# Kernel optimization log

Measured on AMD Instinct MI355X. Metric: run time of the kernel, lower is better.

Reference implementation:

```python
import jax, jax.numpy as jnp
import numpy as np

NEG_SLOPE_ATT = 0.2   # PyG GATConv attention leaky_relu slope
NEG_SLOPE_ACT = 0.01  # F.leaky_relu default between layers


def gat_conv(h, W, a_src, a_dst, b, src, dst, n_nodes):
    """Single-head PyG GATConv (concat, heads=1), self-loops already in src/dst."""
    h = h @ W                                     # [N, out]
    s = h @ a_src                                 # [N] per-node src attention logit
    d = h @ a_dst                                 # [N] per-node dst attention logit
    e = jax.nn.leaky_relu(s[src] + d[dst], negative_slope=NEG_SLOPE_ATT)  # [E']
    # numerically stable segment softmax over edges grouped by dst
    m = jax.ops.segment_max(e, dst, num_segments=n_nodes)
    ex = jnp.exp(e - jax.lax.stop_gradient(m)[dst])
    denom = jax.ops.segment_sum(ex, dst, num_segments=n_nodes)
    alpha = ex / denom[dst]                       # [E']
    out = jax.ops.segment_sum(h[src] * alpha[:, None], dst, num_segments=n_nodes)
    return out + b


def setup_inputs() -> dict:
    key = jax.random.key(0)
    ks = jax.random.split(key, 12)
    N, E, D, H, O, G = 50000, 800000, 128, 128, 64, 256
    x = jax.random.normal(ks[0], (N, D), dtype=jnp.float32)
    edge_index = jax.random.randint(ks[1], (2, E), 0, N, dtype=jnp.int64)
    batch = jnp.sort(jax.random.randint(ks[2], (N,), 0, G, dtype=jnp.int64))
    def glorot(k, shape):
        fan = sum(shape) if len(shape) > 1 else shape[0]
        return jax.random.normal(k, shape, dtype=jnp.float32) * np.float32(np.sqrt(2.0 / fan))
    return {
        "x": x, "edge_index": edge_index, "batch": batch, "n_graphs": G,
        "W1": glorot(ks[3], (D, H)), "a_src1": glorot(ks[4], (H,)), "a_dst1": glorot(ks[5], (H,)),
        "b1": jnp.zeros((H,), dtype=jnp.float32),
        "W2": glorot(ks[6], (H, O)), "a_src2": glorot(ks[7], (O,)), "a_dst2": glorot(ks[8], (O,)),
        "b2": jnp.zeros((O,), dtype=jnp.float32),
    }


def reference(x, edge_index, batch, n_graphs, W1, a_src1, a_dst1, b1, W2, a_src2, a_dst2, b2):
    N = x.shape[0]
    loops = jnp.arange(N, dtype=edge_index.dtype)
    src = jnp.concatenate([edge_index[0], loops])  # add self-loops (GATConv default)
    dst = jnp.concatenate([edge_index[1], loops])
    h = gat_conv(x, W1, a_src1, a_dst1, b1, src, dst, N)
    h = jax.nn.leaky_relu(h, negative_slope=NEG_SLOPE_ACT)  # dropout is identity in eval
    node_emb = gat_conv(h, W2, a_src2, a_dst2, b2, src, dst, N)
    # global_mean_pool
    sums = jax.ops.segment_sum(node_emb, batch, num_segments=n_graphs)
    counts = jax.ops.segment_sum(jnp.ones((N,), dtype=node_emb.dtype), batch, num_segments=n_graphs)
    return sums / jnp.maximum(counts, 1.0)[:, None]
```

## Files before the change

kernel.cpp:

```cpp
#include <hip/hip_runtime.h>

#define NEG_ATT 0.2f
#define NEG_ACT 0.01f

typedef short bf16x8 __attribute__((ext_vector_type(8)));
typedef float f32x4 __attribute__((ext_vector_type(4)));

__device__ __forceinline__ float lrelu(float x, float sl) { return x > 0.0f ? x : x * sl; }

__device__ __forceinline__ unsigned short f2bf(float f) {
  unsigned u = __float_as_uint(f);
  u = u + 0x7FFFu + ((u >> 16) & 1u);
  return (unsigned short)(u >> 16);
}
__device__ __forceinline__ float bf2f(unsigned short h) {
  return __uint_as_float(((unsigned)h) << 16);
}
__device__ __forceinline__ unsigned fenc(float f) {
  unsigned u = __float_as_uint(f);
  return u ^ ((unsigned)((int)u >> 31) | 0x80000000u);
}
__device__ __forceinline__ float fdec(unsigned e) {
  unsigned u = (e & 0x80000000u) ? (e ^ 0x80000000u) : ~e;
  return __uint_as_float(u);
}

#define BIN_CHUNK 4096
#define SLAB_CAP 4096
#define GEMM_LDS 34848

__global__ void prep_w_kernel(const float* __restrict__ W1, const float* __restrict__ W2,
                              unsigned short* __restrict__ w1h, unsigned short* __restrict__ w1l,
                              unsigned short* __restrict__ w2h, unsigned short* __restrict__ w2l,
                              int* __restrict__ bcur, unsigned* __restrict__ maxenc,
                              int NB, int H, int O) {
  int idx = blockIdx.x * 256 + threadIdx.x;
  if (idx < NB) bcur[idx] = 0;
  if (idx == NB) { maxenc[0] = 0u; maxenc[1] = 0u; }
  int n1 = 128 * H;
  const float* W; unsigned short *hi, *lo; int FOUT;
  if (idx < n1) {
    W = W1; hi = w1h; lo = w1l; FOUT = H;
  } else {
    idx -= n1;
    if (idx >= 128 * O) return;
    W = W2; hi = w2h; lo = w2l; FOUT = O;
  }
  int k = idx / FOUT, n = idx % FOUT;
  float w = W[idx];
  unsigned short h = f2bf(w);
  unsigned short l = f2bf(w - bf2f(h));
  int dst = ((k >> 3) * FOUT + n) * 8 + (k & 7);
  hi[dst] = h;
  lo[dst] = l;
}

__device__ __forceinline__ void binA_body(char* smem, const int* __restrict__ src,
                                          const int* __restrict__ dst, int* __restrict__ bcur,
                                          unsigned* __restrict__ pairs, int E, int NB) {
  int* hist = (int*)smem;
  int* cur = hist + 512;
  int tid = threadIdx.x;
  for (int t = tid; t < NB; t += 256) hist[t] = 0;
  __syncthreads();
  int base = blockIdx.x * BIN_CHUNK;
  int s[16], d[16];
#pragma unroll
  for (int i = 0; i < 16; ++i) {
    int idx = base + i * 256 + tid;
    s[i] = 0; d[i] = -1;
    if (idx < E) {
      s[i] = src[idx];
      d[i] = dst[idx];
      atomicAdd(&hist[d[i] >> 7], 1);
    }
  }
  __syncthreads();
  for (int t = tid; t < NB; t += 256) cur[t] = atomicAdd(&bcur[t], hist[t]);
  __syncthreads();
#pragma unroll
  for (int i = 0; i < 16; ++i) {
    if (d[i] >= 0) {
      int b = d[i] >> 7;
      int pos = atomicAdd(&cur[b], 1);
      if (pos < SLAB_CAP)
        pairs[(size_t)b * SLAB_CAP + pos] = (unsigned)s[i] | ((unsigned)(d[i] & 127) << 17);
    }
  }
}

template <int FOUT>
__device__ __forceinline__ void gemm_body(
    char* smem, const float* __restrict__ X, const unsigned short* __restrict__ Wh,
    const unsigned short* __restrict__ Wl,
    const float* __restrict__ asrc, const float* __restrict__ adst,
    unsigned short* __restrict__ Ho, float* __restrict__ So, float* __restrict__ Do,
    unsigned* __restrict__ maxslot, int N, int rowbase) {
  constexpr int NCB = FOUT / 16;
  unsigned short* Ah = (unsigned short*)smem;
  unsigned short* Al = Ah + 64 * 136;
  float* smaxw = (float*)(smem + 2 * 64 * 136 * 2);
  int tid = threadIdx.x;
#pragma unroll
  for (int i = 0; i < 8; ++i) {
    int idx = i * 256 + tid;
    int r = idx >> 5, c4 = (idx & 31) << 2;
    float4 v = make_float4(0.f, 0.f, 0.f, 0.f);
    if (rowbase + r < N) v = *(const float4*)(X + (size_t)(rowbase + r) * 128 + c4);
    ushort4 hv, lv;
    hv.x = f2bf(v.x); lv.x = f2bf(v.x - bf2f(hv.x));
    hv.y = f2bf(v.y); lv.y = f2bf(v.y - bf2f(hv.y));
    hv.z = f2bf(v.z); lv.z = f2bf(v.z - bf2f(hv.z));
    hv.w = f2bf(v.w); lv.w = f2bf(v.w - bf2f(hv.w));
    *(ushort4*)&Ah[r * 136 + c4] = hv;
    *(ushort4*)&Al[r * 136 + c4] = lv;
  }
  __syncthreads();
  int wave = tid >> 6, lane = tid & 63;
  int n15 = lane & 15, bq = lane >> 4;
  int rw = wave * 16;
// ... 43 lines not shown
    }
  }
  float mx = -3e38f;
#pragma unroll
  for (int i = 0; i < 4; ++i) {
    int row = rowbase + rw + 4 * bq + i;
    if (row < N) mx = fmaxf(mx, pS[i]);
  }
#pragma unroll
  for (int off = 32; off; off >>= 1) mx = fmaxf(mx, __shfl_xor(mx, off));
  if (lane == 0) smaxw[wave] = mx;
  __syncthreads();
  if (tid == 0) {
    float m4 = fmaxf(fmaxf(smaxw[0], smaxw[1]), fmaxf(smaxw[2], smaxw[3]));
    atomicMax(maxslot, fenc(m4));
  }
#pragma unroll
  for (int c = 0; c < NCB; ++c)
#pragma unroll
    for (int i = 0; i < 4; ++i)
      Ah[(rw + 4 * bq + i) * 136 + c * 16 + n15] = f2bf(acc[c][i]);
  __syncthreads();
  constexpr int UPT = FOUT / 32;
  int r = tid >> 2, sg = tid & 3;
  if (rowbase + r < N) {
#pragma unroll
    for (int q = 0; q < UPT; ++q) {
      uint4 v = *(uint4*)&Ah[r * 136 + (sg * UPT + q) * 8];
      *(uint4*)(Ho + (size_t)(rowbase + r) * FOUT + (sg * UPT + q) * 8) = v;
    }
  }
}

__global__ __launch_bounds__(256) void binA_gemm_kernel(
    const int* __restrict__ src, const int* __restrict__ dst, int* __restrict__ bcur,
    unsigned* __restrict__ pairs, int E, int NB, int NBA,
    const float* __restrict__ X, const unsigned short* __restrict__ Wh,
    const unsigned short* __restrict__ Wl,
    const float* __restrict__ asrc, const float* __restrict__ adst,
    unsigned short* __restrict__ Ho, float* __restrict__ So, float* __restrict__ Do,
    unsigned* __restrict__ maxslot, int N) {
  extern __shared__ __align__(16) char smem[];
  if (blockIdx.x < (unsigned)NBA)
    binA_body(smem, src, dst, bcur, pairs, E, NB);
  else
    gemm_body<128>(smem, X, Wh, Wl, asrc, adst, Ho, So, Do, maxslot, N,
                   (blockIdx.x - NBA) * 64);
}

template <int FOUT>
__global__ __launch_bounds__(256) void gemm_mfma_kernel(
    const float* __restrict__ X, const unsigned short* __restrict__ Wh,
    const unsigned short* __restrict__ Wl,
    const float* __restrict__ asrc, const float* __restrict__ adst,
    unsigned short* __restrict__ Ho, float* __restrict__ So, float* __restrict__ Do,
    unsigned* __restrict__ maxslot, int N) {
  extern __shared__ __align__(16) char smem[];
  gemm_body<FOUT>(smem, X, Wh, Wl, asrc, adst, Ho, So, Do, maxslot, N, blockIdx.x * 64);
}

__global__ __launch_bounds__(256) void binB_kernel(const unsigned* __restrict__ pairs,
                                                   const int* __restrict__ bcur,
                                                   int2* __restrict__ start2,
                                                   int* __restrict__ ssrc, int N) {
  __shared__ unsigned lp[SLAB_CAP];
  __shared__ int lsorted[SLAB_CAP];
  __shared__ int lcnt[128], lexc[128], lcur[128], stmp[128];
  int b = blockIdx.x, tid = threadIdx.x;
  int dstbase = b << 7;
  int nmax = min(128, N - dstbase);
  int sbase = b * SLAB_CAP;
  int cnt = min(bcur[b], SLAB_CAP);
  if (tid < 128) { lcnt[tid] = 0; lcur[tid] = 0; }
  __syncthreads();
  for (int i = tid; i < cnt; i += 256) {
    unsigned v = pairs[sbase + i];
    lp[i] = v;
    atomicAdd(&lcnt[v >> 17], 1);
  }
  __syncthreads();
  if (tid < 128) stmp[tid] = lcnt[tid];
  __syncthreads();
  for (int off = 1; off < 128; off <<= 1) {
    int t = (tid < 128 && tid >= off) ? stmp[tid - off] : 0;
    __syncthreads();
    if (tid < 128) stmp[tid] += t;
    __syncthreads();
  }
  if (tid < 128) lexc[tid] = stmp[tid] - lcnt[tid];
  __syncthreads();
  if (tid < nmax)
    start2[dstbase + tid] = make_int2(sbase + lexc[tid], sbase + lexc[tid] + lcnt[tid]);
  for (int i = tid; i < cnt; i += 256) {
    unsigned v = lp[i];
    int ld = (int)(v >> 17);
    int r = atomicAdd(&lcur[ld], 1);
    lsorted[lexc[ld] + r] = (int)(v & 0x1FFFFu);
  }
  __syncthreads();
  for (int i = tid; i < cnt; i += 256) ssrc[sbase + i] = lsorted[i];
}

template <int F, bool ACT>
__global__ __launch_bounds__(256) void agg_kernel(
    const unsigned short* __restrict__ Hb, const float* __restrict__ S,
    const float* __restrict__ Dv, const int2* __restrict__ start2,
    const int* __restrict__ ssrc, const float* __restrict__ bias,
    const unsigned* __restrict__ maxenc, float* __restrict__ out, int N) {
  constexpr int VPL = 8;
  constexpr int GL = F / VPL;
  constexpr int GPW = 64 / GL;
  constexpr int GPB = 4 * GPW;
  constexpr int EPL = 64 / GL;
  __shared__ int2 stash[GPB][68];
  int tid = threadIdx.x;
  int wave = tid >> 6, lane = tid & 63;
  int grp = lane / GL, gl = lane % GL;
  int gid = wave * GPW + grp;
  int n = blockIdx.x * GPB + gid;
  if (n >= N) return;
  float dn = Dv[n];
  float M = lrelu(fdec(*maxenc) + dn, NEG_ATT);
  float pself = __expf(lrelu(S[n] + dn, NEG_ATT) - M);
  float acc[VPL];
  {
    uint4 hv = *(const uint4*)(Hb + (size_t)n * F + gl * 8);
    acc[0] = pself * __uint_as_float(hv.x << 16);
    acc[1] = pself * __uint_as_float(hv.x & 0xffff0000u);
    acc[2] = pself * __uint_as_float(hv.y << 16);
    acc[3] = pself * __uint_as_float(hv.y & 0xffff0000u);
    acc[4] = pself * __uint_as_float(hv.z << 16);
    acc[5] = pself * __uint_as_float(hv.z & 0xffff0000u);
    acc[6] = pself * __uint_as_float(hv.w << 16);
    acc[7] = pself * __uint_as_float(hv.w & 0xffff0000u);
  }
  float psum = 0.f;
  int2 se = start2[n];
  int j0 = se.x, j1 = se.y;
  for (int sc = j0; sc < j1; sc += 64) {
    int scnt = min(64, j1 - sc);
    int sj[EPL]; float e[EPL];
#pragma unroll
    for (int q = 0; q < EPL; ++q) {
      int idx = sc + q * GL + gl;
      sj[q] = (idx < j1) ? ssrc[idx] : 0;
    }
#pragma unroll
    for (int q = 0; q < EPL; ++q) {
      int idx = sc + q * GL + gl;
      e[q] = (idx < j1) ? lrelu(S[sj[q]] + dn, NEG_ATT) : 0.f;
    }
#pragma unroll
    for (int q = 0; q < EPL; ++q) {
      int idx = sc + q * GL + gl;
      float p = (idx < j1) ? __expf(e[q] - M) : 0.f;
      psum += p;
      stash[gid][q * GL + gl] = make_int2(sj[q], __float_as_int(p));
    }
#pragma unroll 2
    for (int bb = 0; bb < scnt; bb += 8) {
      int2 sp[8];
      uint4 hv[8];
#pragma unroll
      for (int t = 0; t < 8; ++t)
        if (bb + t < scnt) sp[t] = stash[gid][bb + t];
#pragma unroll
      for (int t = 0; t < 8; ++t)
        if (bb + t < scnt) hv[t] = *(const uint4*)(Hb + (size_t)sp[t].x * F + gl * 8);
#pragma unroll
      for (int t = 0; t < 8; ++t)
        if (bb + t < scnt) {
          float pb = __int_as_float(sp[t].y);
          acc[0] = fmaf(pb, __uint_as_float(hv[t].x << 16), acc[0]);
          acc[1] = fmaf(pb, __uint_as_float(hv[t].x & 0xffff0000u), acc[1]);
          acc[2] = fmaf(pb, __uint_as_float(hv[t].y << 16), acc[2]);
          acc[3] = fmaf(pb, __uint_as_float(hv[t].y & 0xffff0000u), acc[3]);
          acc[4] = fmaf(pb, __uint_as_float(hv[t].z << 16), acc[4]);
          acc[5] = fmaf(pb, __uint_as_float(hv[t].z & 0xffff0000u), acc[5]);
          acc[6] = fmaf(pb, __uint_as_float(hv[t].w << 16), acc[6]);
          acc[7] = fmaf(pb, __uint_as_float(hv[t].w & 0xffff0000u), acc[7]);
        }
    }
  }
#pragma unroll
  for (int off = GL / 2; off; off >>= 1) psum += __shfl_xor(psum, off);
  float inv = 1.0f / (psum + pself);
  float o[VPL];
#pragma unroll
  for (int v = 0; v < VPL; ++v) {
    o[v] = acc[v] * inv + bias[gl * VPL + v];
    if constexpr (ACT) o[v] = lrelu(o[v], NEG_ACT);
  }
  float4 o0 = make_float4(o[0], o[1], o[2], o[3]);
  float4 o1 = make_float4(o[4], o[5], o[6], o[7]);
  *(float4*)(out + (size_t)n * F + gl * VPL) = o0;
  *(float4*)(out + (size_t)n * F + gl * VPL + 4) = o1;
}

__global__ __launch_bounds__(256) void pool_kernel(const float* __restrict__ emb,
                                                   const int* __restrict__ batch,
                                                   float* __restrict__ out, int N) {
  int g = blockIdx.x;
  auto lower = [&](int key) {
    int lo = 0, hi = N;
    while (lo < hi) {
      int mid = (lo + hi) >> 1;
      if (batch[mid] < key) lo = mid + 1; else hi = mid;
    }
    return lo;
  };
  int lo = lower(g), hi = lower(g + 1);
  int c = threadIdx.x & 63, r = threadIdx.x >> 6;
  float s = 0.0f;
  for (int n = lo + r; n < hi; n += 4) s += emb[(size_t)n * 64 + c];
  __shared__ float red[4][64];
  red[r][c] = s;
  __syncthreads();
  if (r == 0) {
    float tot = red[0][c] + red[1][c] + red[2][c] + red[3][c];
    out[g * 64 + c] = tot / fmaxf((float)(hi - lo), 1.0f);
  }
}

extern "C" void kernel_launch(void* const* d_in, const int* in_sizes, int n_in,
                              void* d_out, int out_size, void* d_ws, size_t ws_size,
                              hipStream_t stream) {
  const float* x      = (const float*)d_in[0];
  const int*   ei     = (const int*)d_in[1];
  const int*   batch  = (const int*)d_in[2];
  const float* W1     = (const float*)d_in[4];
  const float* a_src1 = (const float*)d_in[5];
  const float* a_dst1 = (const float*)d_in[6];
  const float* b1     = (const float*)d_in[7];
  const float* W2     = (const float*)d_in[8];
  const float* a_src2 = (const float*)d_in[9];
  const float* a_dst2 = (const float*)d_in[10];
  const float* b2     = (const float*)d_in[11];
  float* out = (float*)d_out;

  const int D = 128, H = 128, O = 64;
  int N = in_sizes[0] / D;
  int E = in_sizes[1] / 2;
  int G = out_size / O;
  const int* src = ei;
  const int* dst = ei + E;
  int NB = (N + 127) >> 7;
  int NBA = (E + BIN_CHUNK - 1) / BIN_CHUNK;

  char* w = (char*)d_ws;
  auto alloc = [&](size_t bytes) -> char* {
    char* p = w;
    w += (bytes + 255) & ~(size_t)255;
    return p;
  };
  unsigned short* h1b = (unsigned short*)alloc((size_t)N * H * 2);
  float* act1  = (float*)alloc((size_t)N * H * 4);
  unsigned short* h2b = (unsigned short*)alloc((size_t)N * O * 2);
  float* emb   = (float*)alloc((size_t)N * O * 4);
  int*      ssrc  = (int*)alloc((size_t)NB * SLAB_CAP * 4);
  unsigned* pairs = (unsigned*)alloc((size_t)NB * SLAB_CAP * 4);
  int2*  start2 = (int2*)alloc((size_t)N * 8);
  int*   bcur   = (int*)alloc(512 * 4);
  float* s1    = (float*)alloc((size_t)N * 4);
  float* d1    = (float*)alloc((size_t)N * 4);
  float* s2    = (float*)alloc((size_t)N * 4);
  float* d2    = (float*)alloc((size_t)N * 4);
  unsigned* maxenc = (unsigned*)alloc(2 * 4);
  unsigned short* w1h = (unsigned short*)alloc((size_t)D * H * 2);
  unsigned short* w1l = (unsigned short*)alloc((size_t)D * H * 2);
  unsigned short* w2h = (unsigned short*)alloc((size_t)H * O * 2);
  unsigned short* w2l = (unsigned short*)alloc((size_t)H * O * 2);

  prep_w_kernel<<<(128 * (H + O) + 255) / 256, 256, 0, stream>>>(
      W1, W2, w1h, w1l, w2h, w2l, bcur, maxenc, NB, H, O);

  int gb = (N + 63) / 64;
  binA_gemm_kernel<<<NBA + gb, 256, GEMM_LDS, stream>>>(
      src, dst, bcur, pairs, E, NB, NBA,
      x, w1h, w1l, a_src1, a_dst1, h1b, s1, d1, maxenc + 0, N);
  binB_kernel<<<NB, 256, 0, stream>>>(pairs, bcur, start2, ssrc, N);
  agg_kernel<128, true><<<(N + 15) / 16, 256, 0, stream>>>(h1b, s1, d1, start2, ssrc, b1,
                                                           maxenc + 0, act1, N);
  gemm_mfma_kernel<64><<<gb, 256, GEMM_LDS, stream>>>(act1, w2h, w2l, a_src2, a_dst2,
                                                      h2b, s2, d2, maxenc + 1, N);
  agg_kernel<64, false><<<(N + 31) / 32, 256, 0, stream>>>(h2b, s2, d2, start2, ssrc, b2,
                                                           maxenc + 1, emb, N);
  pool_kernel<<<G, 256, 0, stream>>>(emb, batch, out, N);
}
```

Before: 142.5 us.

## Fuse all GAT stages into one persistent cooperative kernel with grid syncs

Replaces the seven separate kernel launches (weight prep, binning+GEMM1, bin sort, aggregation 1, GEMM2, aggregation 2, pooling) with a single cooperative mega-kernel. Blocks walk each phase's work items in a grid-stride loop, with grid.sync() between phases and a shared dynamic LDS buffer reused by every phase. The aim is to remove launch overhead and the idle tails between dependent kernels. In exchange it pays six grid-wide barriers and caps the grid at the occupancy-limited resident block count. The __launch_bounds__(256,4) register limit may also hurt the GEMM and aggregation bodies.

```diff
diff --git a/kernel.cpp b/kernel.cpp
--- a/kernel.cpp
+++ b/kernel.cpp
@@ -1,4 +1,7 @@
 #include <hip/hip_runtime.h>
+#include <hip/hip_cooperative_groups.h>
+
+namespace cg = cooperative_groups;
 
 #define NEG_ATT 0.2f
 #define NEG_ACT 0.01f
@@ -27,43 +30,18 @@
 
 #define BIN_CHUNK 4096
 #define SLAB_CAP 4096
-#define GEMM_LDS 34848
-
-__global__ void prep_w_kernel(const float* __restrict__ W1, const float* __restrict__ W2,
-                              unsigned short* __restrict__ w1h, unsigned short* __restrict__ w1l,
-                              unsigned short* __restrict__ w2h, unsigned short* __restrict__ w2l,
-                              int* __restrict__ bcur, unsigned* __restrict__ maxenc,
-                              int NB, int H, int O) {
-  int idx = blockIdx.x * 256 + threadIdx.x;
-  if (idx < NB) bcur[idx] = 0;
-  if (idx == NB) { maxenc[0] = 0u; maxenc[1] = 0u; }
-  int n1 = 128 * H;
-  const float* W; unsigned short *hi, *lo; int FOUT;
-  if (idx < n1) {
-    W = W1; hi = w1h; lo = w1l; FOUT = H;
-  } else {
-    idx -= n1;
-    if (idx >= 128 * O) return;
-    W = W2; hi = w2h; lo = w2l; FOUT = O;
-  }
-  int k = idx / FOUT, n = idx % FOUT;
-  float w = W[idx];
-  unsigned short h = f2bf(w);
-  unsigned short l = f2bf(w - bf2f(h));
-  int dst = ((k >> 3) * FOUT + n) * 8 + (k & 7);
-  hi[dst] = h;
-  lo[dst] = l;
-}
+#define SMEM_BYTES 34848
 
 __device__ __forceinline__ void binA_body(char* smem, const int* __restrict__ src,
                                           const int* __restrict__ dst, int* __restrict__ bcur,
-                                          unsigned* __restrict__ pairs, int E, int NB) {
+                                          unsigned* __restrict__ pairs, int E, int NB,
+                                          int chunk) {
   int* hist = (int*)smem;
   int* cur = hist + 512;
   int tid = threadIdx.x;
   for (int t = tid; t < NB; t += 256) hist[t] = 0;
   __syncthreads();
-  int base = blockIdx.x * BIN_CHUNK;
+  int base = chunk * BIN_CHUNK;
   int s[16], d[16];
 #pragma unroll
   for (int i = 0; i < 16; ++i) {
@@ -195,41 +173,17 @@
   }
 }
 
-__global__ __launch_bounds__(256) void binA_gemm_kernel(
-    const int* __restrict__ src, const int* __restrict__ dst, int* __restrict__ bcur,
-    unsigned* __restrict__ pairs, int E, int NB, int NBA,
-    const float* __restrict__ X, const unsigned short* __restrict__ Wh,
-    const unsigned short* __restrict__ Wl,
-    const float* __restrict__ asrc, const float* __restrict__ adst,
-    unsigned short* __restrict__ Ho, float* __restrict__ So, float* __restrict__ Do,
-    unsigned* __restrict__ maxslot, int N) {
-  extern __shared__ __align__(16) char smem[];
-  if (blockIdx.x < (unsigned)NBA)
-    binA_body(smem, src, dst, bcur, pairs, E, NB);
-  else
-    gemm_body<128>(smem, X, Wh, Wl, asrc, adst, Ho, So, Do, maxslot, N,
-                   (blockIdx.x - NBA) * 64);
-}
-
-template <int FOUT>
-__global__ __launch_bounds__(256) void gemm_mfma_kernel(
-    const float* __restrict__ X, const unsigned short* __restrict__ Wh,
-    const unsigned short* __restrict__ Wl,
-    const float* __restrict__ asrc, const float* __restrict__ adst,
-    unsigned short* __restrict__ Ho, float* __restrict__ So, float* __restrict__ Do,
-    unsigned* __restrict__ maxslot, int N) {
-  extern __shared__ __align__(16) char smem[];
-  gemm_body<FOUT>(smem, X, Wh, Wl, asrc, adst, Ho, So, Do, maxslot, N, blockIdx.x * 64);
-}
-
-__global__ __launch_bounds__(256) void binB_kernel(const unsigned* __restrict__ pairs,
-                                                   const int* __restrict__ bcur,
-                                                   int2* __restrict__ start2,
-                                                   int* __restrict__ ssrc, int N) {
-  __shared__ unsigned lp[SLAB_CAP];
-  __shared__ int lsorted[SLAB_CAP];
-  __shared__ int lcnt[128], lexc[128], lcur[128], stmp[128];
-  int b = blockIdx.x, tid = threadIdx.x;
+__device__ __forceinline__ void binB_body(char* smem, const unsigned* __restrict__ pairs,
+                                          const int* __restrict__ bcur,
+                                          int2* __restrict__ start2,
+                                          int* __restrict__ ssrc, int N, int b) {
+  unsigned* lp = (unsigned*)smem;
+  int* lsorted = (int*)(smem + 16384);
+  int* lcnt = (int*)(smem + 32768);
+  int* lexc = lcnt + 128;
+  int* lcur = lcnt + 256;
+  int* stmp = lcnt + 384;
+  int tid = threadIdx.x;
   int dstbase = b << 7;
   int nmax = min(128, N - dstbase);
   int sbase = b * SLAB_CAP;
@@ -265,22 +219,22 @@
 }
 
 template <int F, bool ACT>
-__global__ __launch_bounds__(256) void agg_kernel(
-    const unsigned short* __restrict__ Hb, const float* __restrict__ S,
+__device__ __forceinline__ void agg_body(
+    char* smem, const unsigned short* __restrict__ Hb, const float* __restrict__ S,
     const float* __restrict__ Dv, const int2* __restrict__ start2,
     const int* __restrict__ ssrc, const float* __restrict__ bias,
-    const unsigned* __restrict__ maxenc, float* __restrict__ out, int N) {
+    const unsigned* __restrict__ maxenc, float* __restrict__ out, int N, int blk) {
   constexpr int VPL = 8;
   constexpr int GL = F / VPL;
   constexpr int GPW = 64 / GL;
   constexpr int GPB = 4 * GPW;
   constexpr int EPL = 64 / GL;
-  __shared__ int2 stash[GPB][68];
+  int2* stash = (int2*)smem;
   int tid = threadIdx.x;
   int wave = tid >> 6, lane = tid & 63;
   int grp = lane / GL, gl = lane % GL;
   int gid = wave * GPW + grp;
-  int n = blockIdx.x * GPB + gid;
+  int n = blk * GPB + gid;
   if (n >= N) return;
   float dn = Dv[n];
   float M = lrelu(fdec(*maxenc) + dn, NEG_ATT);
@@ -318,7 +272,7 @@
       int idx = sc + q * GL + gl;
       float p = (idx < j1) ? __expf(e[q] - M) : 0.f;
       psum += p;
-      stash[gid][q * GL + gl] = make_int2(sj[q], __float_as_int(p));
+      stash[gid * 68 + q * GL + gl] = make_int2(sj[q], __float_as_int(p));
     }
 #pragma unroll 2
     for (int bb = 0; bb < scnt; bb += 8) {
@@ -326,7 +280,7 @@
       uint4 hv[8];
 #pragma unroll
       for (int t = 0; t < 8; ++t)
-        if (bb + t < scnt) sp[t] = stash[gid][bb + t];
+        if (bb + t < scnt) sp[t] = stash[gid * 68 + bb + t];
 #pragma unroll
       for (int t = 0; t < 8; ++t)
         if (bb + t < scnt) hv[t] = *(const uint4*)(Hb + (size_t)sp[t].x * F + gl * 8);
@@ -360,10 +314,10 @@
   *(float4*)(out + (size_t)n * F + gl * VPL + 4) = o1;
 }
 
-__global__ __launch_bounds__(256) void pool_kernel(const float* __restrict__ emb,
-                                                   const int* __restrict__ batch,
-                                                   float* __restrict__ out, int N) {
-  int g = blockIdx.x;
+__device__ __forceinline__ void pool_body(char* smem, const float* __restrict__ emb,
+                                          const int* __restrict__ batch,
+                                          float* __restrict__ out, int N, int g) {
+  float* red = (float*)smem;
   auto lower = [&](int key) {
     int lo = 0, hi = N;
     while (lo < hi) {
@@ -376,12 +330,88 @@
   int c = threadIdx.x & 63, r = threadIdx.x >> 6;
   float s = 0.0f;
   for (int n = lo + r; n < hi; n += 4) s += emb[(size_t)n * 64 + c];
-  __shared__ float red[4][64];
-  red[r][c] = s;
+  red[r * 64 + c] = s;
   __syncthreads();
   if (r == 0) {
-    float tot = red[0][c] + red[1][c] + red[2][c] + red[3][c];
+    float tot = red[0 * 64 + c] + red[1 * 64 + c] + red[2 * 64 + c] + red[3 * 64 + c];
     out[g * 64 + c] = tot / fmaxf((float)(hi - lo), 1.0f);
+  }
+}
+
+__global__ __launch_bounds__(256, 4) void mega_kernel(
+    const int* src, const int* dst, const int* batch, const float* x,
+    const float* W1, const float* a_src1, const float* a_dst1, const float* b1,
+    const float* W2, const float* a_src2, const float* a_dst2, const float* b2,
+    float* out,
+    unsigned short* h1b, float* act1, unsigned short* h2b, float* emb,
+    int* ssrc, unsigned* pairs, int2* start2, int* bcur,
+    float* s1, float* d1, float* s2, float* d2, unsigned* maxenc,
+    unsigned short* w1h, unsigned short* w1l, unsigned short* w2h, unsigned short* w2l,
+    int N, int E, int G, int NB, int NBA, int gb) {
+  extern __shared__ __align__(16) char smem[];
+  cg::grid_group grid = cg::this_grid();
+  const int H = 128, O = 64;
+  int tid = threadIdx.x;
+
+  int total0 = 128 * (H + O);
+  for (int idx0 = blockIdx.x * 256 + tid; idx0 < total0; idx0 += gridDim.x * 256) {
+    int idx = idx0;
+    const float* W; unsigned short *hi, *lo; int FOUT;
+    if (idx < 128 * H) { W = W1; hi = w1h; lo = w1l; FOUT = H; }
+    else { idx -= 128 * H; W = W2; hi = w2h; lo = w2l; FOUT = O; }
+    int k = idx / FOUT, n = idx % FOUT;
+    float wv = W[idx];
+    unsigned short h = f2bf(wv);
+    unsigned short l = f2bf(wv - bf2f(h));
+    int dsti = ((k >> 3) * FOUT + n) * 8 + (k & 7);
+    hi[dsti] = h;
+    lo[dsti] = l;
+  }
+  for (int idx = blockIdx.x * 256 + tid; idx < NB + 2; idx += gridDim.x * 256) {
+    if (idx < NB) bcur[idx] = 0;
+    else maxenc[idx - NB] = 0u;
+  }
+  grid.sync();
+
+  for (int wk = blockIdx.x; wk < NBA + gb; wk += gridDim.x) {
+    if (wk < NBA)
+      binA_body(smem, src, dst, bcur, pairs, E, NB, wk);
+    else
+      gemm_body<128>(smem, x, w1h, w1l, a_src1, a_dst1, h1b, s1, d1, maxenc + 0, N,
+                     (wk - NBA) * 64);
+    __syncthreads();
+  }
+  grid.sync();
+
+  for (int wk = blockIdx.x; wk < NB; wk += gridDim.x) {
+    binB_body(smem, pairs, bcur, start2, ssrc, N, wk);
+    __syncthreads();
+  }
+  grid.sync();
+
+  int nagg1 = (N + 15) / 16;
+  for (int wk = blockIdx.x; wk < nagg1; wk += gridDim.x) {
+    agg_body<128, true>(smem, h1b, s1, d1, start2, ssrc, b1, maxenc + 0, act1, N, wk);
+    __syncthreads();
+  }
+  grid.sync();
+
+  for (int wk = blockIdx.x; wk < gb; wk += gridDim.x) {
+    gemm_body<64>(smem, act1, w2h, w2l, a_src2, a_dst2, h2b, s2, d2, maxenc + 1, N, wk * 64);
+    __syncthreads();
+  }
+  grid.sync();
+
+  int nagg2 = (N + 31) / 32;
+  for (int wk = blockIdx.x; wk < nagg2; wk += gridDim.x) {
+    agg_body<64, false>(smem, h2b, s2, d2, start2, ssrc, b2, maxenc + 1, emb, N, wk);
+    __syncthreads();
+  }
+  grid.sync();
+
+  for (int wk = blockIdx.x; wk < G; wk += gridDim.x) {
+    pool_body(smem, emb, batch, out, N, wk);
+    __syncthreads();
   }
 }
 
@@ -409,6 +439,7 @@
   const int* dst = ei + E;
   int NB = (N + 127) >> 7;
   int NBA = (E + BIN_CHUNK - 1) / BIN_CHUNK;
+  int gb = (N + 63) / 64;
 
   char* w = (char*)d_ws;
   auto alloc = [&](size_t bytes) -> char* {
@@ -434,19 +465,29 @@
   unsigned short* w2h = (unsigned short*)alloc((size_t)H * O * 2);
   unsigned short* w2l = (unsigned short*)alloc((size_t)H * O * 2);
 
-  prep_w_kernel<<<(128 * (H + O) + 255) / 256, 256, 0, stream>>>(
-      W1, W2, w1h, w1l, w2h, w2l, bcur, maxenc, NB, H, O);
-
-  int gb = (N + 63) / 64;
-  binA_gemm_kernel<<<NBA + gb, 256, GEMM_LDS, stream>>>(
-      src, dst, bcur, pairs, E, NB, NBA,
-      x, w1h, w1l, a_src1, a_dst1, h1b, s1, d1, maxenc + 0, N);
-  binB_kernel<<<NB, 256, 0, stream>>>(pairs, bcur, start2, ssrc, N);
-  agg_kernel<128, true><<<(N + 15) / 16, 256, 0, stream>>>(h1b, s1, d1, start2, ssrc, b1,
-                                                           maxenc + 0, act1, N);
-  gemm_mfma_kernel<64><<<gb, 256, GEMM_LDS, stream>>>(act1, w2h, w2l, a_src2, a_dst2,
-                                                      h2b, s2, d2, maxenc + 1, N);
-  agg_kernel<64, false><<<(N + 31) / 32, 256, 0, stream>>>(h2b, s2, d2, start2, ssrc, b2,
-                                                           maxenc + 1, emb, N);
-  pool_kernel<<<G, 256, 0, stream>>>(emb, batch, out, N);
-}
+  int dev = 0;
+  hipGetDevice(&dev);
+  int numCU = 256;
+  hipDeviceGetAttribute(&numCU, hipDeviceAttributeMultiprocessorCount, dev);
+  int occ = 0;
+  hipOccupancyMaxActiveBlocksPerMultiprocessor(&occ, (const void*)mega_kernel, 256,
+                                               SMEM_BYTES);
+  if (occ < 1) occ = 1;
+  long grid = (long)occ * numCU;
+  long maxwork = (N + 15) / 16;
+  if (grid > maxwork) grid = maxwork;
+
+  void* kargs[] = {
+      (void*)&src, (void*)&dst, (void*)&batch, (void*)&x,
+      (void*)&W1, (void*)&a_src1, (void*)&a_dst1, (void*)&b1,
+      (void*)&W2, (void*)&a_src2, (void*)&a_dst2, (void*)&b2,
+      (void*)&out,
+      (void*)&h1b, (void*)&act1, (void*)&h2b, (void*)&emb,
+      (void*)&ssrc, (void*)&pairs, (void*)&start2, (void*)&bcur,
+      (void*)&s1, (void*)&d1, (void*)&s2, (void*)&d2, (void*)&maxenc,
+      (void*)&w1h, (void*)&w1l, (void*)&w2h, (void*)&w2l,
+      (void*)&N, (void*)&E, (void*)&G, (void*)&NB, (void*)&NBA, (void*)&gb};
+
+  hipLaunchCooperativeKernel((void*)mega_kernel, dim3((unsigned)grid), dim3(256),
+                             kargs, SMEM_BYTES, stream);
+}
```

Result: slower. 537.4 us (+277.2%).

## Restructure edge binning into per-chunk cells and fuse pooling into aggregation

Applied to the files above, without the earlier changes.

Edge binning no longer uses a global atomic cursor per destination bucket. Each chunk writes its edges into private fixed-capacity cells (capped at 48 per chunk and bucket) along with a count. The bucket-sort pass is merged with the layer-1 GEMM, and the weight prep and zeroing are merged with the first binning pass, which cuts the launch count and lets independent work overlap. Mean-pool sums are now accumulated with atomics directly in the second aggregation, which drops the embedding buffer write and re-read. The cost is global float atomics on pooled sums, a serial per-cell read loop in binB, and possible edge loss if a cell overflows.

```diff
diff --git a/kernel.cpp b/kernel.cpp
--- a/kernel.cpp
+++ b/kernel.cpp
@@ -26,66 +26,87 @@
 }
 
 #define BIN_CHUNK 4096
+#define CELL_CAP 48
 #define SLAB_CAP 4096
 #define GEMM_LDS 34848
-
-__global__ void prep_w_kernel(const float* __restrict__ W1, const float* __restrict__ W2,
-                              unsigned short* __restrict__ w1h, unsigned short* __restrict__ w1l,
-                              unsigned short* __restrict__ w2h, unsigned short* __restrict__ w2l,
-                              int* __restrict__ bcur, unsigned* __restrict__ maxenc,
-                              int NB, int H, int O) {
-  int idx = blockIdx.x * 256 + threadIdx.x;
-  if (idx < NB) bcur[idx] = 0;
-  if (idx == NB) { maxenc[0] = 0u; maxenc[1] = 0u; }
-  int n1 = 128 * H;
-  const float* W; unsigned short *hi, *lo; int FOUT;
-  if (idx < n1) {
-    W = W1; hi = w1h; lo = w1l; FOUT = H;
-  } else {
-    idx -= n1;
-    if (idx >= 128 * O) return;
-    W = W2; hi = w2h; lo = w2l; FOUT = O;
-  }
-  int k = idx / FOUT, n = idx % FOUT;
-  float w = W[idx];
-  unsigned short h = f2bf(w);
-  unsigned short l = f2bf(w - bf2f(h));
-  int dst = ((k >> 3) * FOUT + n) * 8 + (k & 7);
-  hi[dst] = h;
-  lo[dst] = l;
-}
+#define PREPB 96
 
 __device__ __forceinline__ void binA_body(char* smem, const int* __restrict__ src,
-                                          const int* __restrict__ dst, int* __restrict__ bcur,
-                                          unsigned* __restrict__ pairs, int E, int NB) {
-  int* hist = (int*)smem;
-  int* cur = hist + 512;
+                                          const int* __restrict__ dst,
+                                          unsigned short* __restrict__ cnts,
+                                          unsigned* __restrict__ pairs,
+                                          int E, int NB, int chunk) {
+  int* cur = (int*)smem;
   int tid = threadIdx.x;
-  for (int t = tid; t < NB; t += 256) hist[t] = 0;
-  __syncthreads();
-  int base = blockIdx.x * BIN_CHUNK;
-  int s[16], d[16];
+  for (int t = tid; t < NB; t += 256) cur[t] = 0;
+  __syncthreads();
+  int base = chunk * BIN_CHUNK;
 #pragma unroll
   for (int i = 0; i < 16; ++i) {
     int idx = base + i * 256 + tid;
-    s[i] = 0; d[i] = -1;
     if (idx < E) {
-      s[i] = src[idx];
-      d[i] = dst[idx];
-      atomicAdd(&hist[d[i] >> 7], 1);
-    }
-  }
-  __syncthreads();
-  for (int t = tid; t < NB; t += 256) cur[t] = atomicAdd(&bcur[t], hist[t]);
-  __syncthreads();
-#pragma unroll
-  for (int i = 0; i < 16; ++i) {
-    if (d[i] >= 0) {
-      int b = d[i] >> 7;
+      int sv = src[idx], dv = dst[idx];
+      int b = dv >> 7;
       int pos = atomicAdd(&cur[b], 1);
-      if (pos < SLAB_CAP)
-        pairs[(size_t)b * SLAB_CAP + pos] = (unsigned)s[i] | ((unsigned)(d[i] & 127) << 17);
-    }
+      if (pos < CELL_CAP)
+        pairs[((size_t)chunk * NB + b) * CELL_CAP + pos] =
+            (unsigned)sv | ((unsigned)(dv & 127) << 17);
+    }
+  }
+  __syncthreads();
+  for (int t = tid; t < NB; t += 256)
+    cnts[(size_t)chunk * NB + t] = (unsigned short)min(cur[t], CELL_CAP);
+}
+
+__device__ __forceinline__ void binB_body(char* smem, const unsigned* __restrict__ pairs,
+                                          const unsigned short* __restrict__ cnts,
+                                          int2* __restrict__ start2,
+                                          int* __restrict__ ssrc,
+                                          int N, int NB, int NBA, int b) {
+  unsigned* lp = (unsigned*)smem;
+  int* lcnt = (int*)(smem + SLAB_CAP * 4);
+  int* lexc = lcnt + 128;
+  int* lcur = lexc + 128;
+  int* stmp = lcur + 128;
+  int* misc = stmp + 128;
+  int tid = threadIdx.x;
+  int dstbase = b << 7;
+  int nmax = min(128, N - dstbase);
+  if (tid < 128) { lcnt[tid] = 0; lcur[tid] = 0; }
+  if (tid == 0) misc[0] = 0;
+  __syncthreads();
+  for (int c = tid; c < NBA; c += 256) {
+    int cc = (int)cnts[(size_t)c * NB + b];
+    if (cc) {
+      int lb = atomicAdd(&misc[0], cc);
+      const unsigned* cell = pairs + ((size_t)c * NB + b) * CELL_CAP;
+      for (int i = 0; i < cc; ++i) {
+        unsigned v = cell[i];
+        if (lb + i < SLAB_CAP) lp[lb + i] = v;
+        atomicAdd(&lcnt[(v >> 17) & 127], 1);
+      }
+    }
+  }
+  __syncthreads();
+  if (tid < 128) stmp[tid] = lcnt[tid];
+  __syncthreads();
+  for (int off = 1; off < 128; off <<= 1) {
+    int t = (tid < 128 && tid >= off) ? stmp[tid - off] : 0;
+    __syncthreads();
+    if (tid < 128) stmp[tid] += t;
+    __syncthreads();
+  }
+  if (tid < 128) lexc[tid] = stmp[tid] - lcnt[tid];
+  __syncthreads();
+  int sbase = b * SLAB_CAP;
+  if (tid < nmax)
+    start2[dstbase + tid] = make_int2(sbase + lexc[tid], sbase + lexc[tid] + lcnt[tid]);
+  int total = min(misc[0], SLAB_CAP);
+  for (int i = tid; i < total; i += 256) {
+    unsigned v = lp[i];
+    int ld = (int)((v >> 17) & 127);
+    int r = atomicAdd(&lcur[ld], 1);
+    ssrc[sbase + lexc[ld] + r] = (int)(v & 0x1FFFFu);
   }
 }
 
@@ -195,20 +216,54 @@
   }
 }
 
-__global__ __launch_bounds__(256) void binA_gemm_kernel(
-    const int* __restrict__ src, const int* __restrict__ dst, int* __restrict__ bcur,
-    unsigned* __restrict__ pairs, int E, int NB, int NBA,
-    const float* __restrict__ X, const unsigned short* __restrict__ Wh,
-    const unsigned short* __restrict__ Wl,
-    const float* __restrict__ asrc, const float* __restrict__ adst,
-    unsigned short* __restrict__ Ho, float* __restrict__ So, float* __restrict__ Do,
-    unsigned* __restrict__ maxslot, int N) {
+__global__ __launch_bounds__(256) void u0_kernel(
+    const float* __restrict__ W1, const float* __restrict__ W2,
+    unsigned short* __restrict__ w1h, unsigned short* __restrict__ w1l,
+    unsigned short* __restrict__ w2h, unsigned short* __restrict__ w2l,
+    float* __restrict__ pool, unsigned* __restrict__ maxenc,
+    const int* __restrict__ src, const int* __restrict__ dst,
+    unsigned short* __restrict__ cnts, unsigned* __restrict__ pairs,
+    int E, int NB, int G) {
   extern __shared__ __align__(16) char smem[];
-  if (blockIdx.x < (unsigned)NBA)
-    binA_body(smem, src, dst, bcur, pairs, E, NB);
+  if (blockIdx.x < PREPB) {
+    const int H = 128, O = 64;
+    int tid0 = blockIdx.x * 256 + threadIdx.x;
+    {
+      int idx = tid0;
+      if (idx < 128 * (H + O)) {
+        const float* W; unsigned short *hi, *lo; int FOUT;
+        if (idx < 128 * H) { W = W1; hi = w1h; lo = w1l; FOUT = H; }
+        else { idx -= 128 * H; W = W2; hi = w2h; lo = w2l; FOUT = O; }
+        int k = idx / FOUT, n = idx % FOUT;
+        float wv = W[idx];
+        unsigned short h = f2bf(wv);
+        unsigned short l = f2bf(wv - bf2f(h));
+        int dsti = ((k >> 3) * FOUT + n) * 8 + (k & 7);
+        hi[dsti] = h;
+        lo[dsti] = l;
+      }
+    }
+    if (tid0 < G * 64) pool[tid0] = 0.f;
+    if (tid0 < 2) maxenc[tid0] = 0u;
+  } else {
+    binA_body(smem, src, dst, cnts, pairs, E, NB, blockIdx.x - PREPB);
+  }
+}
+
+__global__ __launch_bounds__(256) void u1_kernel(
+    const unsigned* __restrict__ pairs, const unsigned short* __restrict__ cnts,
+    int2* __restrict__ start2, int* __restrict__ ssrc,
+    const float* __restrict__ x, const unsigned short* __restrict__ w1h,
+    const unsigned short* __restrict__ w1l,
+    const float* __restrict__ a_src1, const float* __restrict__ a_dst1,
+    unsigned short* __restrict__ h1b, float* __restrict__ s1, float* __restrict__ d1,
+    unsigned* __restrict__ maxenc, int N, int NB, int NBA) {
+  extern __shared__ __align__(16) char smem[];
+  if (blockIdx.x < (unsigned)NB)
+    binB_body(smem, pairs, cnts, start2, ssrc, N, NB, NBA, blockIdx.x);
   else
-    gemm_body<128>(smem, X, Wh, Wl, asrc, adst, Ho, So, Do, maxslot, N,
-                   (blockIdx.x - NBA) * 64);
+    gemm_body<128>(smem, x, w1h, w1l, a_src1, a_dst1, h1b, s1, d1, maxenc + 0, N,
+                   (blockIdx.x - NB) * 64);
 }
 
 template <int FOUT>
@@ -222,54 +277,13 @@
   gemm_body<FOUT>(smem, X, Wh, Wl, asrc, adst, Ho, So, Do, maxslot, N, blockIdx.x * 64);
 }
 
-__global__ __launch_bounds__(256) void binB_kernel(const unsigned* __restrict__ pairs,
-                                                   const int* __restrict__ bcur,
-                                                   int2* __restrict__ start2,
-                                                   int* __restrict__ ssrc, int N) {
-  __shared__ unsigned lp[SLAB_CAP];
-  __shared__ int lsorted[SLAB_CAP];
-  __shared__ int lcnt[128], lexc[128], lcur[128], stmp[128];
-  int b = blockIdx.x, tid = threadIdx.x;
-  int dstbase = b << 7;
-  int nmax = min(128, N - dstbase);
-  int sbase = b * SLAB_CAP;
-  int cnt = min(bcur[b], SLAB_CAP);
-  if (tid < 128) { lcnt[tid] = 0; lcur[tid] = 0; }
-  __syncthreads();
-  for (int i = tid; i < cnt; i += 256) {
-    unsigned v = pairs[sbase + i];
-    lp[i] = v;
-    atomicAdd(&lcnt[v >> 17], 1);
-  }
-  __syncthreads();
-  if (tid < 128) stmp[tid] = lcnt[tid];
-  __syncthreads();
-  for (int off = 1; off < 128; off <<= 1) {
-    int t = (tid < 128 && tid >= off) ? stmp[tid - off] : 0;
-    __syncthreads();
-    if (tid < 128) stmp[tid] += t;
-    __syncthreads();
-  }
-  if (tid < 128) lexc[tid] = stmp[tid] - lcnt[tid];
-  __syncthreads();
-  if (tid < nmax)
-    start2[dstbase + tid] = make_int2(sbase + lexc[tid], sbase + lexc[tid] + lcnt[tid]);
-  for (int i = tid; i < cnt; i += 256) {
-    unsigned v = lp[i];
-    int ld = (int)(v >> 17);
-    int r = atomicAdd(&lcur[ld], 1);
-    lsorted[lexc[ld] + r] = (int)(v & 0x1FFFFu);
-  }
-  __syncthreads();
-  for (int i = tid; i < cnt; i += 256) ssrc[sbase + i] = lsorted[i];
-}
-
-template <int F, bool ACT>
+template <int F, bool ACT, bool POOL>
 __global__ __launch_bounds__(256) void agg_kernel(
     const unsigned short* __restrict__ Hb, const float* __restrict__ S,
     const float* __restrict__ Dv, const int2* __restrict__ start2,
     const int* __restrict__ ssrc, const float* __restrict__ bias,
-    const unsigned* __restrict__ maxenc, float* __restrict__ out, int N) {
+    const unsigned* __restrict__ maxenc, float* __restrict__ out,
+    const int* __restrict__ batch, float* __restrict__ pool, int N) {
   constexpr int VPL = 8;
   constexpr int GL = F / VPL;
   constexpr int GPW = 64 / GL;
@@ -354,16 +368,22 @@
     o[v] = acc[v] * inv + bias[gl * VPL + v];
     if constexpr (ACT) o[v] = lrelu(o[v], NEG_ACT);
   }
-  float4 o0 = make_float4(o[0], o[1], o[2], o[3]);
-  float4 o1 = make_float4(o[4], o[5], o[6], o[7]);
-  *(float4*)(out + (size_t)n * F + gl * VPL) = o0;
-  *(float4*)(out + (size_t)n * F + gl * VPL + 4) = o1;
-}
-
-__global__ __launch_bounds__(256) void pool_kernel(const float* __restrict__ emb,
-                                                   const int* __restrict__ batch,
-                                                   float* __restrict__ out, int N) {
-  int g = blockIdx.x;
+  if constexpr (POOL) {
+    int g = batch[n];
+#pragma unroll
+    for (int v = 0; v < VPL; ++v)
+      atomicAdd(&pool[(size_t)g * 64 + gl * VPL + v], o[v]);
+  } else {
+    float4 o0 = make_float4(o[0], o[1], o[2], o[3]);
+    float4 o1 = make_float4(o[4], o[5], o[6], o[7]);
+    *(float4*)(out + (size_t)n * F + gl * VPL) = o0;
+    *(float4*)(out + (size_t)n * F + gl * VPL + 4) = o1;
+  }
+}
+
+__global__ void pool_div_kernel(const float* __restrict__ pool, const int* __restrict__ batch,
+                                float* __restrict__ out, int N) {
+  int g = blockIdx.x, c = threadIdx.x;
   auto lower = [&](int key) {
     int lo = 0, hi = N;
     while (lo < hi) {
@@ -372,17 +392,8 @@
     }
     return lo;
   };
-  int lo = lower(g), hi = lower(g + 1);
-  int c = threadIdx.x & 63, r = threadIdx.x >> 6;
-  float s = 0.0f;
-  for (int n = lo + r; n < hi; n += 4) s += emb[(size_t)n * 64 + c];
-  __shared__ float red[4][64];
-  red[r][c] = s;
-  __syncthreads();
-  if (r == 0) {
-    float tot = red[0][c] + red[1][c] + red[2][c] + red[3][c];
-    out[g * 64 + c] = tot / fmaxf((float)(hi - lo), 1.0f);
-  }
+  int cntg = lower(g + 1) - lower(g);
+  out[g * 64 + c] = pool[g * 64 + c] / fmaxf((float)cntg, 1.0f);
 }
 
 extern "C" void kernel_launch(void* const* d_in, const int* in_sizes, int n_in,
@@ -409,6 +420,7 @@
   const int* dst = ei + E;
   int NB = (N + 127) >> 7;
   int NBA = (E + BIN_CHUNK - 1) / BIN_CHUNK;
+  int gb = (N + 63) / 64;
 
   char* w = (char*)d_ws;
   auto alloc = [&](size_t bytes) -> char* {
@@ -419,34 +431,31 @@
   unsigned short* h1b = (unsigned short*)alloc((size_t)N * H * 2);
   float* act1  = (float*)alloc((size_t)N * H * 4);
   unsigned short* h2b = (unsigned short*)alloc((size_t)N * O * 2);
-  float* emb   = (float*)alloc((size_t)N * O * 4);
   int*      ssrc  = (int*)alloc((size_t)NB * SLAB_CAP * 4);
-  unsigned* pairs = (unsigned*)alloc((size_t)NB * SLAB_CAP * 4);
+  unsigned* pairs = (unsigned*)alloc((size_t)NBA * NB * CELL_CAP * 4);
+  unsigned short* cnts = (unsigned short*)alloc((size_t)NBA * NB * 2);
   int2*  start2 = (int2*)alloc((size_t)N * 8);
-  int*   bcur   = (int*)alloc(512 * 4);
   float* s1    = (float*)alloc((size_t)N * 4);
   float* d1    = (float*)alloc((size_t)N * 4);
   float* s2    = (float*)alloc((size_t)N * 4);
   float* d2    = (float*)alloc((size_t)N * 4);
+  float* pool  = (float*)alloc((size_t)G * O * 4);
   unsigned* maxenc = (unsigned*)alloc(2 * 4);
   unsigned short* w1h = (unsigned short*)alloc((size_t)D * H * 2);
   unsigned short* w1l = (unsigned short*)alloc((size_t)D * H * 2);
   unsigned short* w2h = (unsigned short*)alloc((size_t)H * O * 2);
   unsigned short* w2l = (unsigned short*)alloc((size_t)H * O * 2);
 
-  prep_w_kernel<<<(128 * (H + O) + 255) / 256, 256, 0, stream>>>(
-      W1, W2, w1h, w1l, w2h, w2l, bcur, maxenc, NB, H, O);
-
-  int gb = (N + 63) / 64;
-  binA_gemm_kernel<<<NBA + gb, 256, GEMM_LDS, stream>>>(
-      src, dst, bcur, pairs, E, NB, NBA,
-      x, w1h, w1l, a_src1, a_dst1, h1b, s1, d1, maxenc + 0, N);
-  binB_kernel<<<NB, 256, 0, stream>>>(pairs, bcur, start2, ssrc, N);
-  agg_kernel<128, true><<<(N + 15) / 16, 256, 0, stream>>>(h1b, s1, d1, start2, ssrc, b1,
-                                                           maxenc + 0, act1, N);
+  u0_kernel<<<PREPB + NBA, 256, 2048, stream>>>(W1, W2, w1h, w1l, w2h, w2l, pool, maxenc,
+                                                src, dst, cnts, pairs, E, NB, G);
+  u1_kernel<<<NB + gb, 256, GEMM_LDS, stream>>>(pairs, cnts, start2, ssrc,
+                                                x, w1h, w1l, a_src1, a_dst1,
+                                                h1b, s1, d1, maxenc, N, NB, NBA);
+  agg_kernel<128, true, false><<<(N + 15) / 16, 256, 0, stream>>>(
+      h1b, s1, d1, start2, ssrc, b1, maxenc + 0, act1, nullptr, nullptr, N);
   gemm_mfma_kernel<64><<<gb, 256, GEMM_LDS, stream>>>(act1, w2h, w2l, a_src2, a_dst2,
                                                       h2b, s2, d2, maxenc + 1, N);
-  agg_kernel<64, false><<<(N + 31) / 32, 256, 0, stream>>>(h2b, s2, d2, start2, ssrc, b2,
-                                                           maxenc + 1, emb, N);
-  pool_kernel<<<G, 256, 0, stream>>>(emb, batch, out, N);
-}
+  agg_kernel<64, false, true><<<(N + 31) / 32, 256, 0, stream>>>(
+      h2b, s2, d2, start2, ssrc, b2, maxenc + 1, nullptr, batch, pool, N);
+  pool_div_kernel<<<G, 64, 0, stream>>>(pool, batch, out, N);
+}
```

New measurement: 312.9 us. 120% more time.

## Fuse layer-1 aggregation with layer-2 GEMM and attention logits

Applied to the files above, without the earlier changes.

Layer-1 edge aggregation and the layer-2 projection now run in one kernel. Each 16-node block aggregates its neighbours, applies bias and leaky ReLU, and splits the result into bf16 hi/lo parts in LDS. The same block then multiplies by W2 with MFMA and computes the source/destination logits and the running max. This removes the fp32 act1 buffer round trip through global memory and one kernel launch. In exchange W2 is read from global memory by every block, and the extra LDS and sync may lower occupancy of the memory-bound aggregation.

```diff
diff --git a/kernel.cpp b/kernel.cpp
--- a/kernel.cpp
+++ b/kernel.cpp
@@ -57,13 +57,14 @@
 
 __device__ __forceinline__ void binA_body(char* smem, const int* __restrict__ src,
                                           const int* __restrict__ dst, int* __restrict__ bcur,
-                                          unsigned* __restrict__ pairs, int E, int NB) {
+                                          unsigned* __restrict__ pairs, int E, int NB,
+                                          int chunk) {
   int* hist = (int*)smem;
   int* cur = hist + 512;
   int tid = threadIdx.x;
   for (int t = tid; t < NB; t += 256) hist[t] = 0;
   __syncthreads();
-  int base = blockIdx.x * BIN_CHUNK;
+  int base = chunk * BIN_CHUNK;
   int s[16], d[16];
 #pragma unroll
   for (int i = 0; i < 16; ++i) {
@@ -205,21 +206,10 @@
     unsigned* __restrict__ maxslot, int N) {
   extern __shared__ __align__(16) char smem[];
   if (blockIdx.x < (unsigned)NBA)
-    binA_body(smem, src, dst, bcur, pairs, E, NB);
+    binA_body(smem, src, dst, bcur, pairs, E, NB, blockIdx.x);
   else
     gemm_body<128>(smem, X, Wh, Wl, asrc, adst, Ho, So, Do, maxslot, N,
                    (blockIdx.x - NBA) * 64);
-}
-
-template <int FOUT>
-__global__ __launch_bounds__(256) void gemm_mfma_kernel(
-    const float* __restrict__ X, const unsigned short* __restrict__ Wh,
-    const unsigned short* __restrict__ Wl,
-    const float* __restrict__ asrc, const float* __restrict__ adst,
-    unsigned short* __restrict__ Ho, float* __restrict__ So, float* __restrict__ Do,
-    unsigned* __restrict__ maxslot, int N) {
-  extern __shared__ __align__(16) char smem[];
-  gemm_body<FOUT>(smem, X, Wh, Wl, asrc, adst, Ho, So, Do, maxslot, N, blockIdx.x * 64);
 }
 
 __global__ __launch_bounds__(256) void binB_kernel(const unsigned* __restrict__ pairs,
@@ -262,6 +252,172 @@
   }
   __syncthreads();
   for (int i = tid; i < cnt; i += 256) ssrc[sbase + i] = lsorted[i];
+}
+
+__global__ __launch_bounds__(256) void agg1g2_kernel(
+    const unsigned short* __restrict__ Hb, const float* __restrict__ S,
+    const float* __restrict__ Dv, const int2* __restrict__ start2,
+    const int* __restrict__ ssrc, const float* __restrict__ bias,
+    const unsigned* __restrict__ maxenc,
+    const unsigned short* __restrict__ w2h, const unsigned short* __restrict__ w2l,
+    const float* __restrict__ a_src2, const float* __restrict__ a_dst2,
+    unsigned short* __restrict__ h2b, float* __restrict__ S2, float* __restrict__ D2,
+    unsigned* __restrict__ maxslot2, int N) {
+  constexpr int VPL = 8, GL = 16, GPW = 4, GPB = 16, EPL = 4;
+  __shared__ int2 stash[GPB][68];
+  __shared__ __align__(16) unsigned short A2h[16][136];
+  __shared__ __align__(16) unsigned short A2l[16][136];
+  __shared__ float sdp[2][4][16];
+  int tid = threadIdx.x;
+  int wave = tid >> 6, lane = tid & 63;
+  int grp = lane / GL, gl = lane % GL;
+  int gid = wave * GPW + grp;
+  int nb = blockIdx.x * GPB;
+  int n = nb + gid;
+  bool active = n < N;
+  float o[VPL];
+#pragma unroll
+  for (int v = 0; v < VPL; ++v) o[v] = 0.f;
+  if (active) {
+    float dn = Dv[n];
+    float M = lrelu(fdec(*maxenc) + dn, NEG_ATT);
+    float pself = __expf(lrelu(S[n] + dn, NEG_ATT) - M);
+    float acc[VPL];
+    {
+      uint4 hv = *(const uint4*)(Hb + (size_t)n * 128 + gl * 8);
+      acc[0] = pself * __uint_as_float(hv.x << 16);
+      acc[1] = pself * __uint_as_float(hv.x & 0xffff0000u);
+      acc[2] = pself * __uint_as_float(hv.y << 16);
+      acc[3] = pself * __uint_as_float(hv.y & 0xffff0000u);
+      acc[4] = pself * __uint_as_float(hv.z << 16);
+      acc[5] = pself * __uint_as_float(hv.z & 0xffff0000u);
+      acc[6] = pself * __uint_as_float(hv.w << 16);
+      acc[7] = pself * __uint_as_float(hv.w & 0xffff0000u);
+    }
+    float psum = 0.f;
+    int2 se = start2[n];
+    int j0 = se.x, j1 = se.y;
+    float dn2 = dn;
+    for (int sc = j0; sc < j1; sc += 64) {
+      int scnt = min(64, j1 - sc);
+      int sj[EPL]; float e[EPL];
+#pragma unroll
+      for (int q = 0; q < EPL; ++q) {
+        int idx = sc + q * GL + gl;
+        sj[q] = (idx < j1) ? ssrc[idx] : 0;
+      }
+#pragma unroll
+      for (int q = 0; q < EPL; ++q) {
+        int idx = sc + q * GL + gl;
+        e[q] = (idx < j1) ? lrelu(S[sj[q]] + dn2, NEG_ATT) : 0.f;
+      }
+#pragma unroll
+      for (int q = 0; q < EPL; ++q) {
+        int idx = sc + q * GL + gl;
+        float p = (idx < j1) ? __expf(e[q] - M) : 0.f;
+        psum += p;
+        stash[gid][q * GL + gl] = make_int2(sj[q], __float_as_int(p));
+      }
+#pragma unroll 2
+      for (int bb = 0; bb < scnt; bb += 8) {
+        int2 sp[8];
+        uint4 hv[8];
+#pragma unroll
+        for (int t = 0; t < 8; ++t)
+          if (bb + t < scnt) sp[t] = stash[gid][bb + t];
+#pragma unroll
+        for (int t = 0; t < 8; ++t)
+          if (bb + t < scnt) hv[t] = *(const uint4*)(Hb + (size_t)sp[t].x * 128 + gl * 8);
+#pragma unroll
+        for (int t = 0; t < 8; ++t)
+          if (bb + t < scnt) {
+            float pb = __int_as_float(sp[t].y);
+            acc[0] = fmaf(pb, __uint_as_float(hv[t].x << 16), acc[0]);
+            acc[1] = fmaf(pb, __uint_as_float(hv[t].x & 0xffff0000u), acc[1]);
+            acc[2] = fmaf(pb, __uint_as_float(hv[t].y << 16), acc[2]);
+            acc[3] = fmaf(pb, __uint_as_float(hv[t].y & 0xffff0000u), acc[3]);
+            acc[4] = fmaf(pb, __uint_as_float(hv[t].z << 16), acc[4]);
+            acc[5] = fmaf(pb, __uint_as_float(hv[t].z & 0xffff0000u), acc[5]);
+            acc[6] = fmaf(pb, __uint_as_float(hv[t].w << 16), acc[6]);
+            acc[7] = fmaf(pb, __uint_as_float(hv[t].w & 0xffff0000u), acc[7]);
+          }
+      }
+    }
+#pragma unroll
+    for (int off = GL / 2; off; off >>= 1) psum += __shfl_xor(psum, off);
+    float inv = 1.0f / (psum + pself);
+#pragma unroll
+    for (int v = 0; v < VPL; ++v)
+      o[v] = lrelu(acc[v] * inv + bias[gl * VPL + v], NEG_ACT);
+  }
+  {
+    ushort4 h0, l0, h1, l1;
+    h0.x = f2bf(o[0]); l0.x = f2bf(o[0] - bf2f(h0.x));
+    h0.y = f2bf(o[1]); l0.y = f2bf(o[1] - bf2f(h0.y));
+    h0.z = f2bf(o[2]); l0.z = f2bf(o[2] - bf2f(h0.z));
+    h0.w = f2bf(o[3]); l0.w = f2bf(o[3] - bf2f(h0.w));
+    h1.x = f2bf(o[4]); l1.x = f2bf(o[4] - bf2f(h1.x));
+    h1.y = f2bf(o[5]); l1.y = f2bf(o[5] - bf2f(h1.y));
+    h1.z = f2bf(o[6]); l1.z = f2bf(o[6] - bf2f(h1.z));
+    h1.w = f2bf(o[7]); l1.w = f2bf(o[7] - bf2f(h1.w));
+    *(ushort4*)&A2h[gid][gl * 8] = h0;
+    *(ushort4*)&A2h[gid][gl * 8 + 4] = h1;
+    *(ushort4*)&A2l[gid][gl * 8] = l0;
+    *(ushort4*)&A2l[gid][gl * 8 + 4] = l1;
+  }
+  __syncthreads();
+  int n15 = lane & 15, bq = lane >> 4;
+  int col = wave * 16 + n15;
+  f32x4 g2 = (f32x4){0.f, 0.f, 0.f, 0.f};
+#pragma unroll
+  for (int ks = 0; ks < 4; ++ks) {
+    bf16x8 ah = *(const bf16x8*)&A2h[n15][ks * 32 + bq * 8];
+    bf16x8 al = *(const bf16x8*)&A2l[n15][ks * 32 + bq * 8];
+    bf16x8 bh = *(const bf16x8*)(w2h + ((size_t)(ks * 4 + bq) * 64 + col) * 8);
+    bf16x8 bl = *(const bf16x8*)(w2l + ((size_t)(ks * 4 + bq) * 64 + col) * 8);
+    g2 = __builtin_amdgcn_mfma_f32_16x16x32_bf16(ah, bl, g2, 0, 0, 0);
+    g2 = __builtin_amdgcn_mfma_f32_16x16x32_bf16(al, bh, g2, 0, 0, 0);
+    g2 = __builtin_amdgcn_mfma_f32_16x16x32_bf16(ah, bh, g2, 0, 0, 0);
+  }
+#pragma unroll
+  for (int i = 0; i < 4; ++i) {
+    int node = nb + bq * 4 + i;
+    if (node < N) h2b[(size_t)node * 64 + col] = f2bf(g2[i]);
+  }
+  float av = a_src2[col], bv = a_dst2[col];
+  float ps[4], pd[4];
+#pragma unroll
+  for (int i = 0; i < 4; ++i) { ps[i] = g2[i] * av; pd[i] = g2[i] * bv; }
+#pragma unroll
+  for (int off = 8; off; off >>= 1) {
+#pragma unroll
+    for (int i = 0; i < 4; ++i) {
+      ps[i] += __shfl_xor(ps[i], off);
+      pd[i] += __shfl_xor(pd[i], off);
+    }
+  }
+  if (n15 == 0) {
+#pragma unroll
+    for (int i = 0; i < 4; ++i) {
+      sdp[0][wave][bq * 4 + i] = ps[i];
+      sdp[1][wave][bq * 4 + i] = pd[i];
+    }
+  }
+  __syncthreads();
+  if (wave == 0) {
+    float sS = -3e38f, sD = 0.f;
+    int node = nb + lane;
+    if (lane < 16) {
+      sS = sdp[0][0][lane] + sdp[0][1][lane] + sdp[0][2][lane] + sdp[0][3][lane];
+      sD = sdp[1][0][lane] + sdp[1][1][lane] + sdp[1][2][lane] + sdp[1][3][lane];
+      if (node < N) { S2[node] = sS; D2[node] = sD; }
+      if (node >= N) sS = -3e38f;
+    }
+    float mx = sS;
+#pragma unroll
+    for (int off = 8; off; off >>= 1) mx = fmaxf(mx, __shfl_xor(mx, off));
+    if (lane == 0) atomicMax(maxslot2, fenc(mx));
+  }
 }
 
 template <int F, bool ACT>
@@ -409,6 +565,7 @@
   const int* dst = ei + E;
   int NB = (N + 127) >> 7;
   int NBA = (E + BIN_CHUNK - 1) / BIN_CHUNK;
+  int gb = (N + 63) / 64;
 
   char* w = (char*)d_ws;
   auto alloc = [&](size_t bytes) -> char* {
@@ -417,7 +574,6 @@
     return p;
   };
   unsigned short* h1b = (unsigned short*)alloc((size_t)N * H * 2);
-  float* act1  = (float*)alloc((size_t)N * H * 4);
   unsigned short* h2b = (unsigned short*)alloc((size_t)N * O * 2);
   float* emb   = (float*)alloc((size_t)N * O * 4);
   int*      ssrc  = (int*)alloc((size_t)NB * SLAB_CAP * 4);
@@ -436,16 +592,13 @@
 
   prep_w_kernel<<<(128 * (H + O) + 255) / 256, 256, 0, stream>>>(
       W1, W2, w1h, w1l, w2h, w2l, bcur, maxenc, NB, H, O);
-
-  int gb = (N + 63) / 64;
   binA_gemm_kernel<<<NBA + gb, 256, GEMM_LDS, stream>>>(
       src, dst, bcur, pairs, E, NB, NBA,
       x, w1h, w1l, a_src1, a_dst1, h1b, s1, d1, maxenc + 0, N);
   binB_kernel<<<NB, 256, 0, stream>>>(pairs, bcur, start2, ssrc, N);
-  agg_kernel<128, true><<<(N + 15) / 16, 256, 0, stream>>>(h1b, s1, d1, start2, ssrc, b1,
-                                                           maxenc + 0, act1, N);
-  gemm_mfma_kernel<64><<<gb, 256, GEMM_LDS, stream>>>(act1, w2h, w2l, a_src2, a_dst2,
-                                                      h2b, s2, d2, maxenc + 1, N);
+  agg1g2_kernel<<<(N + 15) / 16, 256, 0, stream>>>(
+      h1b, s1, d1, start2, ssrc, b1, maxenc + 0,
+      w2h, w2l, a_src2, a_dst2, h2b, s2, d2, maxenc + 1, N);
   agg_kernel<64, false><<<(N + 31) / 32, 256, 0, stream>>>(h2b, s2, d2, start2, ssrc, b2,
                                                            maxenc + 1, emb, N);
   pool_kernel<<<G, 256, 0, stream>>>(emb, batch, out, N);
```

Result: no change. 141.2 us (-0.9%).
